# Kernel tuning notes

Hardware: AMD Instinct MI355X
Metric: run time of the kernel (lower is better)

## Reference

```python
import jax, jax.numpy as jnp
import numpy as np

TASK_NUM = 100000
WORKER_NUM = 500
FEATURE_SIZE = 512
CLASS_NUM = 10
ANSWER_NUM = 1000000
HIDDEN = 128
NUM_NODES = TASK_NUM + WORKER_NUM


def setup_inputs() -> dict:
    key = jax.random.key(0)
    ks = jax.random.split(key, 10)
    task_ids = jax.random.randint(ks[0], (ANSWER_NUM,), 0, TASK_NUM, dtype=jnp.int32)
    worker_ids = jax.random.randint(ks[1], (ANSWER_NUM,), 0, WORKER_NUM, dtype=jnp.int32)
    label_ids = jax.random.randint(ks[2], (ANSWER_NUM,), 0, CLASS_NUM, dtype=jnp.int32)
    answers = jnp.stack([task_ids, worker_ids, label_ids], axis=1)  # [A,3]
    return {
        "task_feature": jax.random.normal(ks[3], (TASK_NUM, FEATURE_SIZE), jnp.float32),
        "answers": answers,
        "worker_feature": jax.random.normal(ks[4], (WORKER_NUM, HIDDEN), jnp.float32),
        "W_efc": jax.random.normal(ks[5], (FEATURE_SIZE, HIDDEN), jnp.float32) * 0.05,
        "b_efc": jnp.zeros((HIDDEN,), jnp.float32),
        "W_mean": jax.random.normal(ks[6], (HIDDEN, CLASS_NUM), jnp.float32) * 0.05,
        "b_mean": jnp.zeros((CLASS_NUM,), jnp.float32),
        "W_log_std": jax.random.normal(ks[7], (HIDDEN, CLASS_NUM), jnp.float32) * 0.05,
        "b_log_std": jnp.zeros((CLASS_NUM,), jnp.float32),
        "eps": jax.random.normal(ks[8], (NUM_NODES, CLASS_NUM), jnp.float32),
    }


def _gcn_edges(task_ids, worker_ids):
    # Bipartite edges doubled to be symmetric, plus self-loops (renorm trick).
    row0 = task_ids
    col0 = worker_ids + TASK_NUM
    self_idx = jnp.arange(NUM_NODES, dtype=jnp.int32)
    row = jnp.concatenate([row0, col0, self_idx])
    col = jnp.concatenate([col0, row0, self_idx])
    deg = jax.ops.segment_sum(jnp.ones_like(row, dtype=jnp.float32), row,
                              num_segments=NUM_NODES)
    dinv = jax.lax.rsqrt(deg)  # deg >= 1 thanks to self-loops
    w = dinv[row] * dinv[col]  # [E]
    return row, col, w, row0, col0


def _gcn(x, kernel, bias, row, col, w):
    h = x @ kernel                                   # [N, C]
    msg = h[col] * w[:, None]                        # gather + scale
    return jax.ops.segment_sum(msg, row, num_segments=NUM_NODES) + bias


def reference(task_feature, answers, worker_feature, W_efc, b_efc,
              W_mean, b_mean, W_log_std, b_log_std, eps):
    row, col, w, row0, col0 = _gcn_edges(answers[:, 0], answers[:, 1])
    tf_h = jax.nn.relu(task_feature @ W_efc + b_efc)           # [T, 128]
    x = jnp.concatenate([tf_h, worker_feature], axis=0)        # [N, 128]
    mean = _gcn(x, W_mean, b_mean, row, col, w)                # [N, C]
    log_std = _gcn(x, W_log_std, b_log_std, row, col, w)       # [N, C]
    z = mean + (eps * 0.01) * jnp.exp(log_std)                 # reparam, stddev 0.01
    crowd_out = z[row0] * z[col0]                              # [A, C]
    return crowd_out, mean, log_std
```

## Files before the change

kernel.cpp:

```cpp
#include <hip/hip_runtime.h>

#define T_NUM   100000
#define W_NUM   500
#define N_NODES 100500
#define A_NUM   1000000
#define FEAT    512
#define HID     128
#define CLS     10

#define CSR_STRIDE  40
#define CSRT_STRIDE 2432
#define BM          64
#define HPAD        136
#define NRANGE      8
#define TRNG        (T_NUM / NRANGE)
#define WRNG        64
#define CHUNK       2048
#define NCHUNK      ((A_NUM + CHUNK - 1) / CHUNK)
#define BLD_CAP     64
#define GT_BLKS     ((T_NUM + 255) / 256)

typedef short bf16x8 __attribute__((ext_vector_type(8)));
typedef float f32x4  __attribute__((ext_vector_type(4)));

__device__ __forceinline__ unsigned cvtpk(float lo, float hi) {
    unsigned r;
    asm("v_cvt_pk_bf16_f32 %0, %1, %2" : "=v"(r) : "v"(lo), "v"(hi));
    return r;
}
__device__ __forceinline__ unsigned short f2bf1(float x) {
    return (unsigned short)cvtpk(x, x);
}

__global__ __launch_bounds__(256) void k_build(
        const int* __restrict__ answers, int* __restrict__ cnt,
        int* __restrict__ wcur, int* __restrict__ tick,
        unsigned short* __restrict__ csrW, int* __restrict__ csrT) {
    __shared__ int lcnt[WRNG];
    __shared__ int llist[WRNG * BLD_CAP];
    __shared__ int s_chunk;

    int xcc;
    asm volatile("s_getreg_b32 %0, hwreg(HW_REG_XCC_ID)" : "=s"(xcc));
    const int r   = xcc & (NRANGE - 1);
    const int tlo = r * TRNG, thi = tlo + TRNG;
    const int wlo = r * WRNG;

    for (int i = threadIdx.x; i < WRNG; i += 256) lcnt[i] = 0;

    for (;;) {
        __syncthreads();
        if (threadIdx.x == 0) s_chunk = atomicAdd(&tick[r * 16], 1);
        __syncthreads();
        const int c = s_chunk;
        if (c >= NCHUNK) break;
        const int base = c * CHUNK;
        const int end  = (base + CHUNK < A_NUM) ? base + CHUNK : A_NUM;
        for (int a = base + threadIdx.x; a < end; a += 256) {
            int t = __builtin_nontemporal_load(answers + a * 3);
            int w = __builtin_nontemporal_load(answers + a * 3 + 1);
            if (t >= tlo && t < thi) {
                int p = atomicAdd(&cnt[t], 1);
                if (p < CSR_STRIDE) csrW[(size_t)t * CSR_STRIDE + p] = (unsigned short)w;
            }
            int wr = w - wlo;
            if (wr >= 0 && wr < WRNG && w < W_NUM) {
                int s = atomicAdd(&lcnt[wr], 1);
                if (s < BLD_CAP) llist[wr * BLD_CAP + s] = t;
                else {
                    int q = atomicAdd(&wcur[w * 16], 1);
                    if (q < CSRT_STRIDE) csrT[(size_t)w * CSRT_STRIDE + q] = t;
                }
            }
        }
    }
    __syncthreads();

    for (int wr = threadIdx.x; wr < WRNG; wr += 256) {
        int w = wlo + wr;
        if (w >= W_NUM) continue;
        int c = lcnt[wr];
        if (c > BLD_CAP) c = BLD_CAP;
        if (c == 0) continue;
        int qb = atomicAdd(&wcur[w * 16], c);
        int* dst = csrT + (size_t)w * CSRT_STRIDE;
        for (int j = 0; j < c; j++) {
            int q = qb + j;
            if (q < CSRT_STRIDE) dst[q] = llist[wr * BLD_CAP + j];
        }
    }
}

__global__ void k_prepw(const float* __restrict__ W, unsigned short* __restrict__ Wt,
                        unsigned short* __restrict__ B2t,
                        const float* __restrict__ WF,
                        const float* __restrict__ Wm, const float* __restrict__ Wl,
                        const int* __restrict__ wcur,
                        float* __restrict__ g) {
    int bid = blockIdx.x;
    if (bid < HID) {
        int c = bid;
        for (int k = threadIdx.x; k < FEAT; k += blockDim.x)
            Wt[(size_t)c * FEAT + k] = f2bf1(W[(size_t)k * HID + c]);
    } else if (bid == HID) {
        for (int i = threadIdx.x; i < 32 * HID; i += blockDim.x) {
            int c = i / HID, k = i % HID;
            float v = 0.f;
            if (c < 10)                 v = Wm[k * CLS + c];
            else if (c >= 16 && c < 26) v = Wl[k * CLS + (c - 16)];
            B2t[i] = f2bf1(v);
        }
    } else {
        int idx = (bid - HID - 1) * blockDim.x + threadIdx.x;
        if (idx >= W_NUM * 20) return;
        int w = idx / 20, oc = idx % 20;
        const float* Wc = (oc < 10) ? (Wm + oc) : (Wl + (oc - 10));
        const float* x  = WF + (size_t)w * HID;
        float s = 0.f;
        #pragma unroll 8
        for (int k = 0; k < HID; k++) s = fmaf(x[k], Wc[k * CLS], s);
        float gi = rsqrtf((float)(wcur[w * 16] + 1)) * s;
        g[(size_t)(T_NUM + w) * 20 + oc] = gi;
    }
}

__global__ __launch_bounds__(256, 7) void k_gemm_mfma(
        const float* __restrict__ A, const unsigned short* __restrict__ Wt,
        const float* __restrict__ bias, const unsigned short* __restrict__ B2t,
        const int* __restrict__ cnt, float* __restrict__ g) {
    __shared__ __align__(16) char smem[17408];

    const int tid  = threadIdx.x;
    const int lane = tid & 63;
    const int wv   = tid >> 6;
    const int l15  = lane & 15;
    const int lkg  = lane >> 4;
    const int row  = blockIdx.x * BM + wv * 16 + l15;
    const int rowc = row < T_NUM ? row : T_NUM - 1;
    const float* aptr = A + (size_t)rowc * FEAT + lkg * 8;

    const int scol  = tid >> 1;
    const int shalf = tid & 1;
    const int sswz  = (scol & 7) << 4;
    const int sb0   = (scol * 64 + shalf * 32) ^ sswz;
    const int sb1   = (scol * 64 + shalf * 32 + 16) ^ sswz;
    const unsigned short* sptr = Wt + (size_t)scol * FEAT + shalf * 16;

    const int rswz = (l15 & 7) << 4;

    f32x4 acc[8];
    #pragma unroll
    for (int nt = 0; nt < 8; nt++) acc[nt] = (f32x4){0.f, 0.f, 0.f, 0.f};

    union LU { int4 i; bf16x8 h; };
    union PK { unsigned u[4]; bf16x8 h; };

    float4 ca0 = *(const float4*)(aptr);
    float4 ca1 = *(const float4*)(aptr + 4);
    *(int4*)(smem + sb0) = *(const int4*)(sptr);
    *(int4*)(smem + sb1) = *(const int4*)(sptr + 8);
    __syncthreads();

    for (int ks = 0; ks < 16; ks++) {
        const int k0 = ks * 32;
        float4 na0, na1;
        if (ks < 15) {
            na0 = *(const float4*)(aptr + k0 + 32);
            na1 = *(const float4*)(aptr + k0 + 36);
            char* nb = smem + (((ks + 1) & 1) << 13);
            *(int4*)(nb + sb0) = *(const int4*)(sptr + k0 + 32);
            *(int4*)(nb + sb1) = *(const int4*)(sptr + k0 + 40);
        }
        PK pk;
        pk.u[0] = cvtpk(ca0.x, ca0.y);
        pk.u[1] = cvtpk(ca0.z, ca0.w);
        pk.u[2] = cvtpk(ca1.x, ca1.y);
        pk.u[3] = cvtpk(ca1.z, ca1.w);
        const char* bb = smem + ((ks & 1) << 13);
        #pragma unroll
        for (int nt = 0; nt < 8; nt++) {
            const int boff = ((nt * 16 + l15) * 64 + lkg * 16) ^ rswz;
            LU bu; bu.i = *(const int4*)(bb + boff);
            acc[nt] = __builtin_amdgcn_mfma_f32_16x16x32_bf16(pk.h, bu.h, acc[nt], 0, 0, 0);
        }
        ca0 = na0; ca1 = na1;
        __syncthreads();
    }

    unsigned short* hw = (unsigned short*)smem + wv * 16 * HPAD;
    #pragma unroll
    for (int nt = 0; nt < 8; nt++) {
        float bv = bias[nt * 16 + l15];
        #pragma unroll
        for (int r = 0; r < 4; r++) {
            float h = fmaxf(acc[nt][r] + bv, 0.f);
            hw[(lkg * 4 + r) * HPAD + nt * 16 + l15] = f2bf1(h);
        }
    }

    f32x4 acc2[2];
    acc2[0] = (f32x4){0.f, 0.f, 0.f, 0.f};
    acc2[1] = (f32x4){0.f, 0.f, 0.f, 0.f};
    #pragma unroll
    for (int s = 0; s < 4; s++) {
        LU a2;
        a2.i = *(const int4*)(hw + l15 * HPAD + s * 32 + lkg * 8);
        #pragma unroll
        for (int j = 0; j < 2; j++) {
            LU b2;
            b2.i = *(const int4*)(B2t + (size_t)(j * 16 + l15) * HID + s * 32 + lkg * 8);
            acc2[j] = __builtin_amdgcn_mfma_f32_16x16x32_bf16(a2.h, b2.h, acc2[j], 0, 0, 0);
        }
    }

    if (l15 < 10) {
        #pragma unroll
        for (int r = 0; r < 4; r++) {
            int node = blockIdx.x * BM + wv * 16 + lkg * 4 + r;
            if (node < T_NUM) {
                float di = rsqrtf((float)(cnt[node] + 1));
                g[(size_t)node * 20 + l15]      = di * acc2[0][r];
                g[(size_t)node * 20 + 10 + l15] = di * acc2[1][r];
            }
        }
    }
}

__global__ __launch_bounds__(256) void k_final(
        const int* __restrict__ cnt, const unsigned short* __restrict__ csrW,
        const int* __restrict__ csrT, const int* __restrict__ wcur,
        const float* __restrict__ g,
        const float* __restrict__ b_mean, const float* __restrict__ b_ls,
        const float* __restrict__ eps,
        float* __restrict__ out_mean, float* __restrict__ out_ls,
        float* __restrict__ z) {
    __shared__ float smem[W_NUM * 21];
    const int tid = threadIdx.x;

    if (blockIdx.x >= GT_BLKS) {
        const int w    = blockIdx.x - GT_BLKS;
        const int lane = tid & 63;
        const int wv   = tid >> 6;

        int len = wcur[w * 16];
        int lim = len < CSRT_STRIDE ? len : CSRT_STRIDE;
        const int* lst = csrT + (size_t)w * CSRT_STRIDE;

        float a[20];
        #pragma unroll
        for (int c = 0; c < 20; c++) a[c] = 0.f;

        for (int e = tid; e < lim; e += 256) {
            int t = lst[e];
            const float4* gr = (const float4*)(g + (size_t)t * 20);
            float4 v0 = gr[0], v1 = gr[1], v2 = gr[2], v3 = gr[3], v4 = gr[4];
            a[0] += v0.x; a[1] += v0.y; a[2] += v0.z; a[3] += v0.w;
            a[4] += v1.x; a[5] += v1.y; a[6] += v1.z; a[7] += v1.w;
            a[8] += v2.x; a[9] += v2.y; a[10] += v2.z; a[11] += v2.w;
            a[12] += v3.x; a[13] += v3.y; a[14] += v3.z; a[15] += v3.w;
            a[16] += v4.x; a[17] += v4.y; a[18] += v4.z; a[19] += v4.w;
        }

        #pragma unroll
        for (int off = 32; off; off >>= 1) {
            #pragma unroll
            for (int c = 0; c < 20; c++) a[c] += __shfl_down(a[c], off, 64);
        }

        float* wpart = smem;
        float* fin   = smem + 80;
        if (lane == 0) {
            #pragma unroll
            for (int c = 0; c < 20; c++) wpart[wv * 20 + c] = a[c];
        }
        __syncthreads();

        const int node = T_NUM + w;
        if (tid < 20) {
            float s = wpart[tid] + wpart[20 + tid] + wpart[40 + tid] + wpart[60 + tid];
            float di = rsqrtf((float)(len + 1));
            float gv = g[(size_t)node * 20 + tid];
            if (tid < 10) {
                float m = fmaf(di, s + gv, b_mean[tid]);
                out_mean[(size_t)node * CLS + tid] = m;
                fin[tid] = m;
            } else {
                int c = tid - 10;
                float l = fmaf(di, s + gv, b_ls[c]);
                out_ls[(size_t)node * CLS + c] = l;
                fin[tid] = l;
            }
        }
        __syncthreads();
        if (tid < 10) {
            float m = fin[tid], l = fin[tid + 10];
            z[(size_t)node * CLS + tid] =
                fmaf(eps[(size_t)node * CLS + tid] * 0.01f, expf(l), m);
        }
        return;
    }

    float* gw = smem;
    for (int i = tid; i < W_NUM * 20; i += 256)
        gw[(i / 20) * 21 + (i % 20)] = g[(size_t)T_NUM * 20 + i];
    __syncthreads();

    int t = blockIdx.x * 256 + tid;
    if (t >= T_NUM) return;

    int len = cnt[t];
    int lim = len < CSR_STRIDE ? len : CSR_STRIDE;
    const unsigned short* lst = csrW + (size_t)t * CSR_STRIDE;
    float am[10], al[10];
    #pragma unroll
    for (int c = 0; c < 10; c++) { am[c] = 0.f; al[c] = 0.f; }

    for (int e = 0; e < lim; e++) {
        const float* gg = &gw[lst[e] * 21];
        #pragma unroll
        for (int c = 0; c < 10; c++) {
            am[c] += gg[c];
            al[c] += gg[10 + c];
        }
    }

    float di = rsqrtf((float)(len + 1));
    union { float4 v[5]; float f[20]; } grow;
    const float4* gr = (const float4*)(g + (size_t)t * 20);
    #pragma unroll
    for (int c = 0; c < 5; c++) grow.v[c] = gr[c];

    const float2* ep2 = (const float2*)(eps + (size_t)t * CLS);
    float2* om2 = (float2*)(out_mean + (size_t)t * CLS);
    float2* ol2 = (float2*)(out_ls + (size_t)t * CLS);
    float2* z2  = (float2*)(z + (size_t)t * CLS);
    #pragma unroll
    for (int c = 0; c < 5; c++) {
        float2 ev = ep2[c];
        float m0 = fmaf(di, am[2 * c] + grow.f[2 * c], b_mean[2 * c]);
        float m1 = fmaf(di, am[2 * c + 1] + grow.f[2 * c + 1], b_mean[2 * c + 1]);
        float l0 = fmaf(di, al[2 * c] + grow.f[10 + 2 * c], b_ls[2 * c]);
        float l1 = fmaf(di, al[2 * c + 1] + grow.f[10 + 2 * c + 1], b_ls[2 * c + 1]);
        om2[c] = make_float2(m0, m1);
        ol2[c] = make_float2(l0, l1);
        z2[c]  = make_float2(fmaf(ev.x * 0.01f, expf(l0), m0),
                             fmaf(ev.y * 0.01f, expf(l1), m1));
    }
}

__global__ void k_crowd(const int* __restrict__ answers, const float* __restrict__ z,
                        float* __restrict__ out) {
    int i = blockIdx.x * blockDim.x + threadIdx.x;
    if (i >= A_NUM * 5) return;
    int a = i / 5, c2 = i % 5;
    int t = __builtin_nontemporal_load(answers + a * 3);
    int w = __builtin_nontemporal_load(answers + a * 3 + 1);
    float2 x = *(const float2*)(z + (size_t)t * CLS + c2 * 2);
    float2 y = *(const float2*)(z + (size_t)(T_NUM + w) * CLS + c2 * 2);
    float2 o = make_float2(x.x * y.x, x.y * y.y);
    __builtin_nontemporal_store(o.x, out + (size_t)i * 2);
    __builtin_nontemporal_store(o.y, out + (size_t)i * 2 + 1);
}

extern "C" void kernel_launch(void* const* d_in, const int* in_sizes, int n_in,
                              void* d_out, int out_size, void* d_ws, size_t ws_size,
                              hipStream_t stream) {
    const float* task_feature   = (const float*)d_in[0];
    const int*   answers        = (const int*)d_in[1];
    const float* worker_feature = (const float*)d_in[2];
    const float* W_efc          = (const float*)d_in[3];
    const float* b_efc          = (const float*)d_in[4];
    const float* W_mean         = (const float*)d_in[5];
    const float* b_mean         = (const float*)d_in[6];
    const float* W_ls           = (const float*)d_in[7];
    const float* b_ls           = (const float*)d_in[8];
    const float* eps            = (const float*)d_in[9];

    float* out       = (float*)d_out;
    float* out_crowd = out;
    float* out_mean  = out + (size_t)A_NUM * CLS;
    float* out_ls    = out_mean + (size_t)N_NODES * CLS;

    char* ws = (char*)d_ws;
    int* cnt              = (int*)ws;
    int* wcur             = (int*)(ws + 402432);
    int* tick             = (int*)(ws + 434432);
    unsigned short* csrW  = (unsigned short*)(ws + 434944);
    unsigned short* Wt    = (unsigned short*)(ws + 8434944);
    unsigned short* B2t   = (unsigned short*)(ws + 8566016);
    int* csrT             = (int*)(ws + 8574208);
    float* g              = (float*)(ws + 13438208);
    float* z              = (float*)(ws + 21478208);

    hipMemsetAsync(ws, 0, 434944, stream);

    k_build<<<2048, 256, 0, stream>>>(answers, cnt, wcur, tick, csrW, csrT);
    k_prepw<<<HID + 1 + (W_NUM * 20 + 255) / 256, 256, 0, stream>>>(
        W_efc, Wt, B2t, worker_feature, W_mean, W_ls, wcur, g);
    k_gemm_mfma<<<(T_NUM + BM - 1) / BM, 256, 0, stream>>>(
        task_feature, Wt, b_efc, B2t, cnt, g);
    k_final<<<GT_BLKS + W_NUM, 256, 0, stream>>>(
        cnt, csrW, csrT, wcur, g, b_mean, b_ls, eps, out_mean, out_ls, z);
    k_crowd<<<(A_NUM * 5 + 255) / 256, 256, 0, stream>>>(answers, z, out_crowd);
}
```

Baseline: 193.2 us.

## Make build blocks sweep all ranges and deepen GEMM A-prefetch to two steps

```diff
diff --git a/kernel.cpp b/kernel.cpp
--- a/kernel.cpp
+++ b/kernel.cpp
@@ -17,7 +17,8 @@
 #define WRNG        64
 #define CHUNK       2048
 #define NCHUNK      ((A_NUM + CHUNK - 1) / CHUNK)
-#define BLD_CAP     64
+#define BLD_NBLK    512
+#define BLD_CAP     88
 #define GT_BLKS     ((T_NUM + 255) / 256)
 
 typedef short bf16x8 __attribute__((ext_vector_type(8)));
@@ -39,55 +40,61 @@
     __shared__ int lcnt[WRNG];
     __shared__ int llist[WRNG * BLD_CAP];
     __shared__ int s_chunk;
+    const int tid = threadIdx.x;
 
     int xcc;
     asm volatile("s_getreg_b32 %0, hwreg(HW_REG_XCC_ID)" : "=s"(xcc));
-    const int r   = xcc & (NRANGE - 1);
-    const int tlo = r * TRNG, thi = tlo + TRNG;
-    const int wlo = r * WRNG;
-
-    for (int i = threadIdx.x; i < WRNG; i += 256) lcnt[i] = 0;
-
-    for (;;) {
-        __syncthreads();
-        if (threadIdx.x == 0) s_chunk = atomicAdd(&tick[r * 16], 1);
-        __syncthreads();
-        const int c = s_chunk;
-        if (c >= NCHUNK) break;
-        const int base = c * CHUNK;
-        const int end  = (base + CHUNK < A_NUM) ? base + CHUNK : A_NUM;
-        for (int a = base + threadIdx.x; a < end; a += 256) {
-            int t = __builtin_nontemporal_load(answers + a * 3);
-            int w = __builtin_nontemporal_load(answers + a * 3 + 1);
-            if (t >= tlo && t < thi) {
-                int p = atomicAdd(&cnt[t], 1);
-                if (p < CSR_STRIDE) csrW[(size_t)t * CSR_STRIDE + p] = (unsigned short)w;
-            }
-            int wr = w - wlo;
-            if (wr >= 0 && wr < WRNG && w < W_NUM) {
-                int s = atomicAdd(&lcnt[wr], 1);
-                if (s < BLD_CAP) llist[wr * BLD_CAP + s] = t;
-                else {
-                    int q = atomicAdd(&wcur[w * 16], 1);
-                    if (q < CSRT_STRIDE) csrT[(size_t)w * CSRT_STRIDE + q] = t;
+    const int r0 = xcc & (NRANGE - 1);
+
+    for (int rr = 0; rr < NRANGE; rr++) {
+        const int re  = (r0 + rr) & (NRANGE - 1);
+        const int tlo = re * TRNG, thi = tlo + TRNG;
+        const int wlo = re * WRNG;
+
+        for (int i = tid; i < WRNG; i += 256) lcnt[i] = 0;
+
+        for (;;) {
+            __syncthreads();
+            if (tid == 0) s_chunk = atomicAdd(&tick[re * 16], 1);
+            __syncthreads();
+            const int c = s_chunk;
+            if (c >= NCHUNK) break;
+            const int base = c * CHUNK;
+            const int end  = (base + CHUNK < A_NUM) ? base + CHUNK : A_NUM;
+            for (int a = base + tid; a < end; a += 256) {
+                int t = __builtin_nontemporal_load(answers + a * 3);
+                int w = __builtin_nontemporal_load(answers + a * 3 + 1);
+                if (t >= tlo && t < thi) {
+                    int p = atomicAdd(&cnt[t], 1);
+                    if (p < CSR_STRIDE)
+                        csrW[(size_t)t * CSR_STRIDE + p] = (unsigned short)w;
+                }
+                int wr = w - wlo;
+                if (wr >= 0 && wr < WRNG && w < W_NUM) {
+                    int s = atomicAdd(&lcnt[wr], 1);
+                    if (s < BLD_CAP) llist[wr * BLD_CAP + s] = t;
+                    else {
+                        int q = atomicAdd(&wcur[w * 16], 1);
+                        if (q < CSRT_STRIDE)
+                            csrT[(size_t)w * CSRT_STRIDE + q] = t;
+                    }
                 }
             }
         }
-    }
-    __syncthreads();
-
-    for (int wr = threadIdx.x; wr < WRNG; wr += 256) {
-        int w = wlo + wr;
-        if (w >= W_NUM) continue;
-        int c = lcnt[wr];
-        if (c > BLD_CAP) c = BLD_CAP;
-        if (c == 0) continue;
-        int qb = atomicAdd(&wcur[w * 16], c);
-        int* dst = csrT + (size_t)w * CSRT_STRIDE;
-        for (int j = 0; j < c; j++) {
-            int q = qb + j;
-            if (q < CSRT_STRIDE) dst[q] = llist[wr * BLD_CAP + j];
-        }
+        for (int wr = tid; wr < WRNG; wr += 256) {
+            int w = wlo + wr;
+            if (w >= W_NUM) continue;
+            int c = lcnt[wr];
+            if (c > BLD_CAP) c = BLD_CAP;
+            if (c == 0) continue;
+            int qb = atomicAdd(&wcur[w * 16], c);
+            int* dst = csrT + (size_t)w * CSRT_STRIDE;
+            for (int j = 0; j < c; j++) {
+                int q = qb + j;
+                if (q < CSRT_STRIDE) dst[q] = llist[wr * BLD_CAP + j];
+            }
+        }
+        __syncthreads();
     }
 }
 
@@ -155,37 +162,49 @@
     union LU { int4 i; bf16x8 h; };
     union PK { unsigned u[4]; bf16x8 h; };
 
-    float4 ca0 = *(const float4*)(aptr);
-    float4 ca1 = *(const float4*)(aptr + 4);
+    f32x4 A00 = __builtin_nontemporal_load((const f32x4*)(aptr));
+    f32x4 A01 = __builtin_nontemporal_load((const f32x4*)(aptr + 4));
+    f32x4 A10 = __builtin_nontemporal_load((const f32x4*)(aptr + 32));
+    f32x4 A11 = __builtin_nontemporal_load((const f32x4*)(aptr + 36));
     *(int4*)(smem + sb0) = *(const int4*)(sptr);
     *(int4*)(smem + sb1) = *(const int4*)(sptr + 8);
     __syncthreads();
 
-    for (int ks = 0; ks < 16; ks++) {
-        const int k0 = ks * 32;
-        float4 na0, na1;
-        if (ks < 15) {
-            na0 = *(const float4*)(aptr + k0 + 32);
-            na1 = *(const float4*)(aptr + k0 + 36);
-            char* nb = smem + (((ks + 1) & 1) << 13);
-            *(int4*)(nb + sb0) = *(const int4*)(sptr + k0 + 32);
-            *(int4*)(nb + sb1) = *(const int4*)(sptr + k0 + 40);
-        }
-        PK pk;
-        pk.u[0] = cvtpk(ca0.x, ca0.y);
-        pk.u[1] = cvtpk(ca0.z, ca0.w);
-        pk.u[2] = cvtpk(ca1.x, ca1.y);
-        pk.u[3] = cvtpk(ca1.z, ca1.w);
-        const char* bb = smem + ((ks & 1) << 13);
-        #pragma unroll
-        for (int nt = 0; nt < 8; nt++) {
-            const int boff = ((nt * 16 + l15) * 64 + lkg * 16) ^ rswz;
-            LU bu; bu.i = *(const int4*)(bb + boff);
-            acc[nt] = __builtin_amdgcn_mfma_f32_16x16x32_bf16(pk.h, bu.h, acc[nt], 0, 0, 0);
-        }
-        ca0 = na0; ca1 = na1;
-        __syncthreads();
-    }
+#define GSTEP(AR0, AR1, BUF, NEXTBUF, KS)                                       \
+    {                                                                           \
+        const int k0 = (KS) * 32;                                               \
+        if ((KS) < 15) {                                                        \
+            char* nb = smem + ((NEXTBUF) << 13);                                \
+            *(int4*)(nb + sb0) = *(const int4*)(sptr + k0 + 32);                \
+            *(int4*)(nb + sb1) = *(const int4*)(sptr + k0 + 40);                \
+        }                                                                       \
+        f32x4 n0 = {0.f, 0.f, 0.f, 0.f}, n1 = {0.f, 0.f, 0.f, 0.f};             \
+        if ((KS) < 14) {                                                        \
+            n0 = __builtin_nontemporal_load((const f32x4*)(aptr + k0 + 64));    \
+            n1 = __builtin_nontemporal_load((const f32x4*)(aptr + k0 + 68));    \
+        }                                                                       \
+        PK pk;                                                                  \
+        pk.u[0] = cvtpk(AR0[0], AR0[1]);                                        \
+        pk.u[1] = cvtpk(AR0[2], AR0[3]);                                        \
+        pk.u[2] = cvtpk(AR1[0], AR1[1]);                                        \
+        pk.u[3] = cvtpk(AR1[2], AR1[3]);                                        \
+        const char* bb = smem + ((BUF) << 13);                                  \
+        _Pragma("unroll")                                                       \
+        for (int nt = 0; nt < 8; nt++) {                                        \
+            const int boff = ((nt * 16 + l15) * 64 + lkg * 16) ^ rswz;          \
+            LU bu; bu.i = *(const int4*)(bb + boff);                            \
+            acc[nt] = __builtin_amdgcn_mfma_f32_16x16x32_bf16(pk.h, bu.h,       \
+                                                              acc[nt], 0, 0, 0);\
+        }                                                                       \
+        if ((KS) < 14) { AR0 = n0; AR1 = n1; }                                  \
+        __syncthreads();                                                        \
+    }
+
+    for (int ks2 = 0; ks2 < 16; ks2 += 2) {
+        GSTEP(A00, A01, 0, 1, ks2);
+        GSTEP(A10, A11, 1, 0, ks2 + 1);
+    }
+#undef GSTEP
 
     unsigned short* hw = (unsigned short*)smem + wv * 16 * HPAD;
     #pragma unroll
@@ -394,7 +413,7 @@
 
     hipMemsetAsync(ws, 0, 434944, stream);
 
-    k_build<<<2048, 256, 0, stream>>>(answers, cnt, wcur, tick, csrW, csrT);
+    k_build<<<BLD_NBLK, 256, 0, stream>>>(answers, cnt, wcur, tick, csrW, csrT);
     k_prepw<<<HID + 1 + (W_NUM * 20 + 255) / 256, 256, 0, stream>>>(
         W_efc, Wt, B2t, worker_feature, W_mean, W_ls, wcur, g);
     k_gemm_mfma<<<(T_NUM + BM - 1) / BM, 256, 0, stream>>>(
```

Result: slower. 263.5 us (+36.4%).
